# Kernel optimization log

Hardware: AMD Instinct MI355X
Metric: run time of the kernel (lower is better)

The kernel has to match this reference:

```python
import jax, jax.numpy as jnp
import numpy as np

LEVELS = 16
FEAT_DIM = 2
N_MIN = 16
GROWTH = 1.5
TABLE_SIZE = 524288  # 2**19
B = 16

# NGP-style 2D spatial-hash primes (the repo's _fast_hash_2d is external; this
# is the standard instant-ngp construction with a per-level seed xor).
P1 = np.uint32(2654435761)
P2 = np.uint32(805459861)


def _seeds() -> np.ndarray:
    # Same splitmix-like seed derivation as the torch module, truncated to the
    # low 32 bits since hashing is done in uint32 arithmetic.
    cA = 15485907386658061715
    cB = 11400714819323198485
    M64 = (1 << 64) - 1
    return np.array([(cA ^ ((l * cB) & M64)) & 0xFFFFFFFF for l in range(LEVELS)],
                    dtype=np.uint32)


def _hash2d(ix, iy, seed, table_size):
    h = (ix.astype(jnp.uint32) * P1) ^ (iy.astype(jnp.uint32) * P2) ^ seed
    return (h % jnp.uint32(table_size)).astype(jnp.int32)


def setup_inputs() -> dict:
    key = jax.random.key(0)
    k1, k2, k3 = jax.random.split(key, 3)
    # global crop offsets inside a 1024px tile (crop is 256px)
    x0 = jax.random.uniform(k1, (B,), dtype=jnp.float32) * 768.0
    y0 = jax.random.uniform(k2, (B,), dtype=jnp.float32) * 768.0
    tables = jax.random.uniform(k3, (TABLE_SIZE, FEAT_DIM), dtype=jnp.float32,
                                minval=-0.01, maxval=0.01)
    seeds = jnp.asarray(_seeds())  # uint32 [L]
    return {"x0": x0, "y0": y0, "tables": tables, "seeds": seeds,
            "memorized_crop_size": 256, "complete_tile_size": 1024}


def reference(x0, y0, tables, seeds, memorized_crop_size, complete_tile_size):
    H = W = int(memorized_crop_size)
    L, F = LEVELS, FEAT_DIM
    Bn = x0.shape[0]
    N = H * W
    table_size = tables.shape[0]

    # per-level grid resolutions N_l = round(n_min * growth**l)
    Ns = np.array([round(N_MIN * GROWTH ** l) for l in range(L)], dtype=np.float32)
    scales = jnp.asarray(Ns / float(complete_tile_size))  # [L]

    xs = jnp.arange(H, dtype=jnp.float32)
    yy, xx = jnp.meshgrid(xs, xs, indexing='ij')          # [H,W]
    pxf = (xx[None] + x0[:, None, None]).reshape(Bn, N)   # [B,N] global px coords
    pyf = (yy[None] + y0[:, None, None]).reshape(Bn, N)

    xyn_x = pxf[:, None, :] * scales[None, :, None]       # [B,L,N]
    xyn_y = pyf[:, None, :] * scales[None, :, None]
    ix0 = jnp.floor(xyn_x).astype(jnp.int32)
    iy0 = jnp.floor(xyn_y).astype(jnp.int32)
    fx = (xyn_x - ix0)[..., None]                          # [B,L,N,1]
    fy = (xyn_y - iy0)[..., None]

    seed = seeds[None, :, None]                            # broadcast over B,N
    f00 = tables[_hash2d(ix0,     iy0,     seed, table_size)]  # [B,L,N,F]
    f10 = tables[_hash2d(ix0 + 1, iy0,     seed, table_size)]
    f01 = tables[_hash2d(ix0,     iy0 + 1, seed, table_size)]
    f11 = tables[_hash2d(ix0 + 1, iy0 + 1, seed, table_size)]

    enc = ((1.0 - fx) * (1.0 - fy) * f00 + fx * (1.0 - fy) * f10
           + (1.0 - fx) * fy * f01 + fx * fy * f11)        # [B,L,N,F]

    enc = enc.transpose(0, 2, 1, 3).reshape(Bn, H, W, L * F)  # [B,H,W,L*F]
    return enc.transpose(0, 3, 1, 2)                           # [B,L*F,H,W]
```

## Files before the change

kernel.cpp:

```cpp
#include <hip/hip_runtime.h>
#include <math.h>

#define LEVELS 16
#define FEAT 2

__constant__ float c_Ns[LEVELS] = {
    16.f, 24.f, 36.f, 54.f, 81.f, 122.f, 182.f, 273.f,
    410.f, 615.f, 923.f, 1384.f, 2076.f, 3114.f, 4671.f, 7006.f
};

#define P1 2654435761u
#define P2 805459861u

template <bool POW2_TABLE, bool POW2_W>
__global__ __launch_bounds__(256) void hashenc_kernel(
    const float* __restrict__ x0,
    const float* __restrict__ y0,
    const float2* __restrict__ tables,
    const unsigned int* __restrict__ seeds,
    const int* __restrict__ tile_ptr,
    float* __restrict__ out,
    int N,
    int W,
    int wshift,
    unsigned int tsize,
    unsigned int tmask)
{
    const int pix = blockIdx.x * blockDim.x + threadIdx.x;
    if (pix >= N) return;
    const int b = blockIdx.y;

    int i, j;
    if (POW2_W) {
        i = pix >> wshift;
        j = pix & (W - 1);
    } else {
        i = pix / W;
        j = pix - i * W;
    }

    const int tile = *tile_ptr;
    const float tilef = (float)tile;
    float sc[LEVELS];
    if ((tile & (tile - 1)) == 0) {
        const float inv_tile = 1.0f / tilef;
#pragma unroll
        for (int l = 0; l < LEVELS; ++l) sc[l] = c_Ns[l] * inv_tile;
    } else {
#pragma unroll
        for (int l = 0; l < LEVELS; ++l) sc[l] = c_Ns[l] / tilef;
    }

    const float px = (float)j + x0[b];
    const float py = (float)i + y0[b];

    float* outb = out + (size_t)b * (size_t)(LEVELS * FEAT) * (size_t)N + pix;

#pragma unroll
    for (int l = 0; l < LEVELS; ++l) {
        const float s = sc[l];
        const float xs = px * s;
        const float ys = py * s;
        const float fx0 = floorf(xs);
        const float fy0 = floorf(ys);
        const float fx = xs - fx0;
        const float fy = ys - fy0;
        const unsigned int ux = (unsigned int)(int)fx0;
        const unsigned int uy = (unsigned int)(int)fy0;

        const unsigned int sd = seeds[l];
        const unsigned int ax0 = ux * P1;
        const unsigned int ax1 = ax0 + P1;
        const unsigned int ay0 = (uy * P2) ^ sd;
        const unsigned int ay1 = (uy * P2 + P2) ^ sd;

        unsigned int i00, i10, i01, i11;
        if (POW2_TABLE) {
            i00 = (ax0 ^ ay0) & tmask;
            i10 = (ax1 ^ ay0) & tmask;
            i01 = (ax0 ^ ay1) & tmask;
            i11 = (ax1 ^ ay1) & tmask;
        } else {
            i00 = (ax0 ^ ay0) % tsize;
            i10 = (ax1 ^ ay0) % tsize;
            i01 = (ax0 ^ ay1) % tsize;
            i11 = (ax1 ^ ay1) % tsize;
        }

        const float2 f00 = tables[i00];
        const float2 f10 = tables[i10];
        const float2 f01 = tables[i01];
        const float2 f11 = tables[i11];

        const float omx = 1.0f - fx;
        const float omy = 1.0f - fy;
        const float w00 = omx * omy;
        const float w10 = fx * omy;
        const float w01 = omx * fy;
        const float w11 = fx * fy;

        const float e0 = w00 * f00.x + w10 * f10.x + w01 * f01.x + w11 * f11.x;
        const float e1 = w00 * f00.y + w10 * f10.y + w01 * f01.y + w11 * f11.y;

        __builtin_nontemporal_store(e0, outb + (size_t)(2 * l) * (size_t)N);
        __builtin_nontemporal_store(e1, outb + (size_t)(2 * l + 1) * (size_t)N);
    }
}

extern "C" void kernel_launch(void* const* d_in, const int* in_sizes, int n_in,
                              void* d_out, int out_size, void* d_ws, size_t ws_size,
                              hipStream_t stream) {
    const float* x0 = (const float*)d_in[0];
    const float* y0 = (const float*)d_in[1];
    const float2* tables = (const float2*)d_in[2];
    const unsigned int* seeds = (const unsigned int*)d_in[3];
    const int* tile_ptr = (const int*)d_in[5];

    const int Bn = in_sizes[0];
    const unsigned int tsize = (unsigned int)(in_sizes[2] / FEAT);
    const int N = out_size / (Bn * LEVELS * FEAT);
    const int W = (int)(sqrt((double)N) + 0.5);
    int wshift = 0;
    while ((1 << wshift) < W) ++wshift;

    float* out = (float*)d_out;

    dim3 grid((N + 255) / 256, Bn);
    dim3 block(256);

    const bool pow2_table = (tsize & (tsize - 1)) == 0;
    const bool pow2_w = (W & (W - 1)) == 0;

    if (pow2_table && pow2_w) {
        hashenc_kernel<true, true><<<grid, block, 0, stream>>>(
            x0, y0, tables, seeds, tile_ptr, out, N, W, wshift, tsize, tsize - 1u);
    } else if (pow2_table) {
        hashenc_kernel<true, false><<<grid, block, 0, stream>>>(
            x0, y0, tables, seeds, tile_ptr, out, N, W, wshift, tsize, tsize - 1u);
    } else if (pow2_w) {
        hashenc_kernel<false, true><<<grid, block, 0, stream>>>(
            x0, y0, tables, seeds, tile_ptr, out, N, W, wshift, tsize, 0u);
    } else {
        hashenc_kernel<false, false><<<grid, block, 0, stream>>>(
            x0, y0, tables, seeds, tile_ptr, out, N, W, wshift, tsize, 0u);
    }
}
```

Measured before the change: 255.7 us.

## Software-pipeline table gathers in double-buffered groups of four levels

```diff
diff --git a/kernel.cpp b/kernel.cpp
--- a/kernel.cpp
+++ b/kernel.cpp
@@ -11,6 +11,60 @@
 
 #define P1 2654435761u
 #define P2 805459861u
+
+#define LOADG(G, BUF)                                                          \
+  {                                                                            \
+    _Pragma("unroll") for (int k = 0; k < 4; ++k) {                            \
+      const int l = (G) * 4 + k;                                               \
+      const float s = sc[l];                                                   \
+      const float xs = px * s, ys = py * s;                                    \
+      const float fx0f = floorf(xs), fy0f = floorf(ys);                        \
+      fxb[BUF][k] = xs - fx0f;                                                 \
+      fyb[BUF][k] = ys - fy0f;                                                 \
+      const unsigned int ux = (unsigned int)(int)fx0f;                         \
+      const unsigned int uy = (unsigned int)(int)fy0f;                         \
+      const unsigned int sd = sds[l];                                          \
+      const unsigned int ax0 = ux * P1;                                        \
+      const unsigned int ax1 = ax0 + P1;               \
+      const unsigned int ay0 = (uy * P2) ^ sd;                                 \
+      const unsigned int ay1 = (uy * P2 + P2) ^ sd;                            \
+      unsigned int i00, i10, i01, i11;                                         \
+      if (POW2_TABLE) {                                                        \
+        i00 = (ax0 ^ ay0) & tmask;                                             \
+        i10 = (ax1 ^ ay0) & tmask;                                             \
+        i01 = (ax0 ^ ay1) & tmask;                                             \
+        i11 = (ax1 ^ ay1) & tmask;                                             \
+      } else {                                                                 \
+        i00 = (ax0 ^ ay0) % tsize;                                             \
+        i10 = (ax1 ^ ay0) % tsize;                                             \
+        i01 = (ax0 ^ ay1) % tsize;                                             \
+        i11 = (ax1 ^ ay1) % tsize;                                             \
+      }                                                                        \
+      fb[BUF][k][0] = tables[i00];                                             \
+      fb[BUF][k][1] = tables[i10];                                             \
+      fb[BUF][k][2] = tables[i01];                                             \
+      fb[BUF][k][3] = tables[i11];                                             \
+    }                                                                          \
+  }
+
+#define MATHG(G, BUF)                                                          \
+  {                                                                            \
+    _Pragma("unroll") for (int k = 0; k < 4; ++k) {                            \
+      const int l = (G) * 4 + k;                                               \
+      const float fx = fxb[BUF][k], fy = fyb[BUF][k];                          \
+      const float omx = 1.0f - fx, omy = 1.0f - fy;                            \
+      const float w00 = omx * omy, w10 = fx * omy;                             \
+      const float w01 = omx * fy, w11 = fx * fy;                               \
+      const float2 f00 = fb[BUF][k][0], f10 = fb[BUF][k][1];                   \
+      const float2 f01 = fb[BUF][k][2], f11 = fb[BUF][k][3];                   \
+      const float e0 = w00 * f00.x + w10 * f10.x + w01 * f01.x + w11 * f11.x;  \
+      const float e1 = w00 * f00.y + w10 * f10.y + w01 * f01.y + w11 * f11.y;  \
+      __builtin_nontemporal_store(e0, outb + (size_t)(2 * l) * (size_t)N);     \
+      __builtin_nontemporal_store(e1, outb + (size_t)(2 * l + 1) * (size_t)N); \
+    }                                                                          \
+  }
+
+#define FENCE() __builtin_amdgcn_sched_barrier(0)
 
 template <bool POW2_TABLE, bool POW2_W>
 __global__ __launch_bounds__(256) void hashenc_kernel(
@@ -39,6 +93,10 @@
         j = pix - i * W;
     }
 
+    unsigned int sds[LEVELS];
+#pragma unroll
+    for (int l = 0; l < LEVELS; ++l) sds[l] = seeds[l];
+
     const int tile = *tile_ptr;
     const float tilef = (float)tile;
     float sc[LEVELS];
@@ -56,55 +114,20 @@
 
     float* outb = out + (size_t)b * (size_t)(LEVELS * FEAT) * (size_t)N + pix;
 
-#pragma unroll
-    for (int l = 0; l < LEVELS; ++l) {
-        const float s = sc[l];
-        const float xs = px * s;
-        const float ys = py * s;
-        const float fx0 = floorf(xs);
-        const float fy0 = floorf(ys);
-        const float fx = xs - fx0;
-        const float fy = ys - fy0;
-        const unsigned int ux = (unsigned int)(int)fx0;
-        const unsigned int uy = (unsigned int)(int)fy0;
+    float2 fb[2][4][4];
+    float fxb[2][4], fyb[2][4];
 
-        const unsigned int sd = seeds[l];
-        const unsigned int ax0 = ux * P1;
-        const unsigned int ax1 = ax0 + P1;
-        const unsigned int ay0 = (uy * P2) ^ sd;
-        const unsigned int ay1 = (uy * P2 + P2) ^ sd;
-
-        unsigned int i00, i10, i01, i11;
-        if (POW2_TABLE) {
-            i00 = (ax0 ^ ay0) & tmask;
-            i10 = (ax1 ^ ay0) & tmask;
-            i01 = (ax0 ^ ay1) & tmask;
-            i11 = (ax1 ^ ay1) & tmask;
-        } else {
-            i00 = (ax0 ^ ay0) % tsize;
-            i10 = (ax1 ^ ay0) % tsize;
-            i01 = (ax0 ^ ay1) % tsize;
-            i11 = (ax1 ^ ay1) % tsize;
-        }
-
-        const float2 f00 = tables[i00];
-        const float2 f10 = tables[i10];
-        const float2 f01 = tables[i01];
-        const float2 f11 = tables[i11];
-
-        const float omx = 1.0f - fx;
-        const float omy = 1.0f - fy;
-        const float w00 = omx * omy;
-        const float w10 = fx * omy;
-        const float w01 = omx * fy;
-        const float w11 = fx * fy;
-
-        const float e0 = w00 * f00.x + w10 * f10.x + w01 * f01.x + w11 * f11.x;
-        const float e1 = w00 * f00.y + w10 * f10.y + w01 * f01.y + w11 * f11.y;
-
-        __builtin_nontemporal_store(e0, outb + (size_t)(2 * l) * (size_t)N);
-        __builtin_nontemporal_store(e1, outb + (size_t)(2 * l + 1) * (size_t)N);
-    }
+    LOADG(0, 0)
+    LOADG(1, 1)
+    FENCE();
+    MATHG(0, 0)
+    LOADG(2, 0)
+    FENCE();
+    MATHG(1, 1)
+    LOADG(3, 1)
+    FENCE();
+    MATHG(2, 0)
+    MATHG(3, 1)
 }
 
 extern "C" void kernel_launch(void* const* d_in, const int* in_sizes, int n_in,
```

Result: slower. 263.4 us (+3.0%).

## Stage coarse-level hash table entries in LDS per row-block, prefetch fine levels

Applied to the files above, without the earlier changes.

```diff
diff --git a/kernel.cpp b/kernel.cpp
--- a/kernel.cpp
+++ b/kernel.cpp
@@ -3,6 +3,9 @@
 
 #define LEVELS 16
 #define FEAT 2
+#define NLDSL 12
+#define LDS_CAP 2560
+#define CNT_CAP 768
 
 __constant__ float c_Ns[LEVELS] = {
     16.f, 24.f, 36.f, 54.f, 81.f, 122.f, 182.f, 273.f,
@@ -11,6 +14,159 @@
 
 #define P1 2654435761u
 #define P2 805459861u
+
+template <bool POW2_TABLE>
+__device__ __forceinline__ unsigned hash2d(unsigned ux, unsigned uy, unsigned sd,
+                                           unsigned tsize, unsigned tmask) {
+    const unsigned h = (ux * P1) ^ (uy * P2) ^ sd;
+    return POW2_TABLE ? (h & tmask) : (h % tsize);
+}
+
+template <bool POW2_TABLE>
+__global__ __launch_bounds__(256) void hashenc_lds_kernel(
+    const float* __restrict__ x0v,
+    const float* __restrict__ y0v,
+    const float2* __restrict__ tables,
+    const unsigned int* __restrict__ seeds,
+    const int* __restrict__ tile_ptr,
+    float* __restrict__ out,
+    int N,
+    int bpr,
+    unsigned int tsize,
+    unsigned int tmask)
+{
+    __shared__ float2 ltab[LDS_CAP];
+
+    const int tid = threadIdx.x;
+    const int b = blockIdx.y;
+    const int row = blockIdx.x / bpr;
+    const int j0 = (blockIdx.x - row * bpr) * 256;
+    const int j = j0 + tid;
+
+    const int tile = *tile_ptr;
+    const float tilef = (float)tile;
+    float sc[LEVELS];
+    if ((tile & (tile - 1)) == 0) {
+        const float it = 1.0f / tilef;
+#pragma unroll
+        for (int l = 0; l < LEVELS; ++l) sc[l] = c_Ns[l] * it;
+    } else {
+#pragma unroll
+        for (int l = 0; l < LEVELS; ++l) sc[l] = c_Ns[l] / tilef;
+    }
+
+    const float xb = x0v[b];
+    const float px = (float)j + xb;
+    const float py = (float)row + y0v[b];
+    const float pxl = (float)j0 + xb;
+    const float pxr = (float)(j0 + 255) + xb;
+
+    float ffx[LEVELS - NLDSL], ffy[LEVELS - NLDSL];
+    float2 fr[LEVELS - NLDSL][4];
+#pragma unroll
+    for (int k = 0; k < LEVELS - NLDSL; ++k) {
+        const int l = NLDSL + k;
+        const float s = sc[l];
+        const float xsf = px * s, ysf = py * s;
+        const float fx0 = floorf(xsf), fy0 = floorf(ysf);
+        ffx[k] = xsf - fx0;
+        ffy[k] = ysf - fy0;
+        const unsigned ux = (unsigned)(int)fx0;
+        const unsigned uy = (unsigned)(int)fy0;
+        const unsigned sd = seeds[l];
+        fr[k][0] = tables[hash2d<POW2_TABLE>(ux,      uy,      sd, tsize, tmask)];
+        fr[k][1] = tables[hash2d<POW2_TABLE>(ux + 1u, uy,      sd, tsize, tmask)];
+        fr[k][2] = tables[hash2d<POW2_TABLE>(ux,      uy + 1u, sd, tsize, tmask)];
+        fr[k][3] = tables[hash2d<POW2_TABLE>(ux + 1u, uy + 1u, sd, tsize, tmask)];
+    }
+    __builtin_amdgcn_sched_barrier(0);
+
+    {
+        int run = 0;
+#pragma unroll
+        for (int l = 0; l < NLDSL; ++l) {
+            const float s = sc[l];
+            const int x0i = (int)floorf(pxl * s);
+            const int x1i = (int)floorf(pxr * s);
+            const int iy0 = (int)floorf(py * s);
+            const int xlen = x1i - x0i + 2;
+            const int cnt = 2 * xlen;
+            if (cnt <= CNT_CAP && run + cnt <= LDS_CAP) {
+                const unsigned sd = seeds[l];
+                for (int t = tid; t < cnt; t += 256) {
+                    const int dy = (t >= xlen) ? 1 : 0;
+                    const int xo = t - dy * xlen;
+                    const unsigned ux = (unsigned)(x0i + xo);
+                    const unsigned uy = (unsigned)(iy0 + dy);
+                    ltab[run + t] = tables[hash2d<POW2_TABLE>(ux, uy, sd, tsize, tmask)];
+                }
+                run += cnt;
+            }
+        }
+    }
+    __syncthreads();
+
+    float* outb = out + (size_t)b * (size_t)(LEVELS * FEAT) * (size_t)N
+                      + (size_t)(row * (bpr * 256) + j0 + tid);
+
+#pragma unroll
+    for (int k = 0; k < LEVELS - NLDSL; ++k) {
+        const int l = NLDSL + k;
+        const float fx = ffx[k], fy = ffy[k];
+        const float omx = 1.0f - fx, omy = 1.0f - fy;
+        const float w00 = omx * omy, w10 = fx * omy;
+        const float w01 = omx * fy, w11 = fx * fy;
+        const float2 f00 = fr[k][0], f10 = fr[k][1];
+        const float2 f01 = fr[k][2], f11 = fr[k][3];
+        const float e0 = w00 * f00.x + w10 * f10.x + w01 * f01.x + w11 * f11.x;
+        const float e1 = w00 * f00.y + w10 * f10.y + w01 * f01.y + w11 * f11.y;
+        __builtin_nontemporal_store(e0, outb + (size_t)(2 * l) * (size_t)N);
+        __builtin_nontemporal_store(e1, outb + (size_t)(2 * l + 1) * (size_t)N);
+    }
+
+    {
+        int run = 0;
+#pragma unroll
+        for (int l = 0; l < NLDSL; ++l) {
+            const float s = sc[l];
+            const int x0i = (int)floorf(pxl * s);
+            const int x1i = (int)floorf(pxr * s);
+            const int xlen = x1i - x0i + 2;
+            const int cnt = 2 * xlen;
+            const bool inlds = (cnt <= CNT_CAP && run + cnt <= LDS_CAP);
+
+            const float xsf = px * s, ysf = py * s;
+            const float fx0 = floorf(xsf), fy0 = floorf(ysf);
+            const float fx = xsf - fx0, fy = ysf - fy0;
+
+            float2 f00, f10, f01, f11;
+            if (inlds) {
+                const int a = run + ((int)fx0 - x0i);
+                f00 = ltab[a];
+                f10 = ltab[a + 1];
+                f01 = ltab[a + xlen];
+                f11 = ltab[a + xlen + 1];
+                run += cnt;
+            } else {
+                const unsigned ux = (unsigned)(int)fx0;
+                const unsigned uy = (unsigned)(int)fy0;
+                const unsigned sd = seeds[l];
+                f00 = tables[hash2d<POW2_TABLE>(ux,      uy,      sd, tsize, tmask)];
+                f10 = tables[hash2d<POW2_TABLE>(ux + 1u, uy,      sd, tsize, tmask)];
+                f01 = tables[hash2d<POW2_TABLE>(ux,      uy + 1u, sd, tsize, tmask)];
+                f11 = tables[hash2d<POW2_TABLE>(ux + 1u, uy + 1u, sd, tsize, tmask)];
+            }
+
+            const float omx = 1.0f - fx, omy = 1.0f - fy;
+            const float w00 = omx * omy, w10 = fx * omy;
+            const float w01 = omx * fy, w11 = fx * fy;
+            const float e0 = w00 * f00.x + w10 * f10.x + w01 * f01.x + w11 * f11.x;
+            const float e1 = w00 * f00.y + w10 * f10.y + w01 * f01.y + w11 * f11.y;
+            __builtin_nontemporal_store(e0, outb + (size_t)(2 * l) * (size_t)N);
+            __builtin_nontemporal_store(e1, outb + (size_t)(2 * l + 1) * (size_t)N);
+        }
+    }
+}
 
 template <bool POW2_TABLE, bool POW2_W>
 __global__ __launch_bounds__(256) void hashenc_kernel(
@@ -20,32 +176,24 @@
     const unsigned int* __restrict__ seeds,
     const int* __restrict__ tile_ptr,
     float* __restrict__ out,
-    int N,
-    int W,
-    int wshift,
-    unsigned int tsize,
-    unsigned int tmask)
+    int N, int W, int wshift,
+    unsigned int tsize, unsigned int tmask)
 {
     const int pix = blockIdx.x * blockDim.x + threadIdx.x;
     if (pix >= N) return;
     const int b = blockIdx.y;
 
     int i, j;
-    if (POW2_W) {
-        i = pix >> wshift;
-        j = pix & (W - 1);
-    } else {
-        i = pix / W;
-        j = pix - i * W;
-    }
+    if (POW2_W) { i = pix >> wshift; j = pix & (W - 1); }
+    else        { i = pix / W;       j = pix - i * W;   }
 
     const int tile = *tile_ptr;
     const float tilef = (float)tile;
     float sc[LEVELS];
     if ((tile & (tile - 1)) == 0) {
-        const float inv_tile = 1.0f / tilef;
-#pragma unroll
-        for (int l = 0; l < LEVELS; ++l) sc[l] = c_Ns[l] * inv_tile;
+        const float it = 1.0f / tilef;
+#pragma unroll
+        for (int l = 0; l < LEVELS; ++l) sc[l] = c_Ns[l] * it;
     } else {
 #pragma unroll
         for (int l = 0; l < LEVELS; ++l) sc[l] = c_Ns[l] / tilef;
@@ -53,55 +201,26 @@
 
     const float px = (float)j + x0[b];
     const float py = (float)i + y0[b];
-
     float* outb = out + (size_t)b * (size_t)(LEVELS * FEAT) * (size_t)N + pix;
 
 #pragma unroll
     for (int l = 0; l < LEVELS; ++l) {
         const float s = sc[l];
-        const float xs = px * s;
-        const float ys = py * s;
-        const float fx0 = floorf(xs);
-        const float fy0 = floorf(ys);
-        const float fx = xs - fx0;
-        const float fy = ys - fy0;
-        const unsigned int ux = (unsigned int)(int)fx0;
-        const unsigned int uy = (unsigned int)(int)fy0;
-
-        const unsigned int sd = seeds[l];
-        const unsigned int ax0 = ux * P1;
-        const unsigned int ax1 = ax0 + P1;
-        const unsigned int ay0 = (uy * P2) ^ sd;
-        const unsigned int ay1 = (uy * P2 + P2) ^ sd;
-
-        unsigned int i00, i10, i01, i11;
-        if (POW2_TABLE) {
-            i00 = (ax0 ^ ay0) & tmask;
-            i10 = (ax1 ^ ay0) & tmask;
-            i01 = (ax0 ^ ay1) & tmask;
-            i11 = (ax1 ^ ay1) & tmask;
-        } else {
-            i00 = (ax0 ^ ay0) % tsize;
-            i10 = (ax1 ^ ay0) % tsize;
-            i01 = (ax0 ^ ay1) % tsize;
-            i11 = (ax1 ^ ay1) % tsize;
-        }
-
-        const float2 f00 = tables[i00];
-        const float2 f10 = tables[i10];
-        const float2 f01 = tables[i01];
-        const float2 f11 = tables[i11];
-
-        const float omx = 1.0f - fx;
-        const float omy = 1.0f - fy;
-        const float w00 = omx * omy;
-        const float w10 = fx * omy;
-        const float w01 = omx * fy;
-        const float w11 = fx * fy;
-
+        const float xs = px * s, ys = py * s;
+        const float fx0 = floorf(xs), fy0 = floorf(ys);
+        const float fx = xs - fx0, fy = ys - fy0;
+        const unsigned ux = (unsigned)(int)fx0;
+        const unsigned uy = (unsigned)(int)fy0;
+        const unsigned sd = seeds[l];
+        const float2 f00 = tables[hash2d<POW2_TABLE>(ux,      uy,      sd, tsize, tmask)];
+        const float2 f10 = tables[hash2d<POW2_TABLE>(ux + 1u, uy,      sd, tsize, tmask)];
+        const float2 f01 = tables[hash2d<POW2_TABLE>(ux,      uy + 1u, sd, tsize, tmask)];
+        const float2 f11 = tables[hash2d<POW2_TABLE>(ux + 1u, uy + 1u, sd, tsize, tmask)];
+        const float omx = 1.0f - fx, omy = 1.0f - fy;
+        const float w00 = omx * omy, w10 = fx * omy;
+        const float w01 = omx * fy, w11 = fx * fy;
         const float e0 = w00 * f00.x + w10 * f10.x + w01 * f01.x + w11 * f11.x;
         const float e1 = w00 * f00.y + w10 * f10.y + w01 * f01.y + w11 * f11.y;
-
         __builtin_nontemporal_store(e0, outb + (size_t)(2 * l) * (size_t)N);
         __builtin_nontemporal_store(e1, outb + (size_t)(2 * l + 1) * (size_t)N);
     }
@@ -120,28 +239,35 @@
     const unsigned int tsize = (unsigned int)(in_sizes[2] / FEAT);
     const int N = out_size / (Bn * LEVELS * FEAT);
     const int W = (int)(sqrt((double)N) + 0.5);
+    float* out = (float*)d_out;
+    const bool pow2_table = (tsize & (tsize - 1)) == 0;
+
+    if (W >= 256 && (W % 256) == 0) {
+        const int bpr = W / 256;
+        dim3 grid(N / 256, Bn);
+        if (pow2_table)
+            hashenc_lds_kernel<true><<<grid, 256, 0, stream>>>(
+                x0, y0, tables, seeds, tile_ptr, out, N, bpr, tsize, tsize - 1u);
+        else
+            hashenc_lds_kernel<false><<<grid, 256, 0, stream>>>(
+                x0, y0, tables, seeds, tile_ptr, out, N, bpr, tsize, 0u);
+        return;
+    }
+
     int wshift = 0;
     while ((1 << wshift) < W) ++wshift;
-
-    float* out = (float*)d_out;
-
     dim3 grid((N + 255) / 256, Bn);
-    dim3 block(256);
-
-    const bool pow2_table = (tsize & (tsize - 1)) == 0;
     const bool pow2_w = (W & (W - 1)) == 0;
-
-    if (pow2_table && pow2_w) {
-        hashenc_kernel<true, true><<<grid, block, 0, stream>>>(
+    if (pow2_table && pow2_w)
+        hashenc_kernel<true, true><<<grid, 256, 0, stream>>>(
             x0, y0, tables, seeds, tile_ptr, out, N, W, wshift, tsize, tsize - 1u);
-    } else if (pow2_table) {
-        hashenc_kernel<true, false><<<grid, block, 0, stream>>>(
+    else if (pow2_table)
+        hashenc_kernel<true, false><<<grid, 256, 0, stream>>>(
             x0, y0, tables, seeds, tile_ptr, out, N, W, wshift, tsize, tsize - 1u);
-    } else if (pow2_w) {
-        hashenc_kernel<false, true><<<grid, block, 0, stream>>>(
+    else if (pow2_w)
+        hashenc_kernel<false, true><<<grid, 256, 0, stream>>>(
             x0, y0, tables, seeds, tile_ptr, out, N, W, wshift, tsize, 0u);
-    } else {
-        hashenc_kernel<false, false><<<grid, block, 0, stream>>>(
+    else
+        hashenc_kernel<false, false><<<grid, 256, 0, stream>>>(
             x0, y0, tables, seeds, tile_ptr, out, N, W, wshift, tsize, 0u);
-    }
-}
+}
```

Measured after the change: 265.0 us. 3.6% more time.
